# Kernel tuning notes

Hardware: AMD Instinct MI355X
Metric: run time of the kernel (lower is better)

Reference implementation:

```python
import jax, jax.numpy as jnp
import numpy as np

H = 768            # hidden_size
IMG_H = 1024       # image_hidden_size
NH = 12            # num_heads
NKV = 1            # num_kv_heads (MQA)
HD = H // NH       # head_dim = 64
FF = 4 * H         # intermediate_size = 3072
EPS = 1e-5


def layernorm(x, g, b):
    m = jnp.mean(x, axis=-1, keepdims=True)
    v = jnp.mean(jnp.square(x - m), axis=-1, keepdims=True)
    return (x - m) * jax.lax.rsqrt(v + EPS) * g + b


def setup_inputs() -> dict:
    key = jax.random.key(0)
    ks = jax.random.split(key, 12)
    B, NQ, NIMG = 8, 256, 4096
    s = 0.02
    return {
        "hidden_states": jax.random.normal(ks[0], (B, NQ, H), jnp.float32),
        "image_features": jax.random.normal(ks[1], (B, NIMG, IMG_H), jnp.float32),
        # norm_image_pre
        "ln_img_g": jnp.ones((IMG_H,), jnp.float32),
        "ln_img_b": jnp.zeros((IMG_H,), jnp.float32),
        # image_bottleneck (bias=False)
        "W_bottle": jax.random.normal(ks[2], (IMG_H, H), jnp.float32) * s,
        # norm_hidden
        "ln_h_g": jnp.ones((H,), jnp.float32),
        "ln_h_b": jnp.zeros((H,), jnp.float32),
        # to_q
        "Wq": jax.random.normal(ks[3], (H, H), jnp.float32) * s,
        "bq": jnp.zeros((H,), jnp.float32),
        # to_kv: out = num_kv_heads * head_dim * 2
        "Wkv": jax.random.normal(ks[4], (H, 2 * NKV * HD), jnp.float32) * s,
        "bkv": jnp.zeros((2 * NKV * HD,), jnp.float32),
        # to_out
        "Wo": jax.random.normal(ks[5], (H, H), jnp.float32) * s,
        "bo": jnp.zeros((H,), jnp.float32),
        # attn_out_norm
        "ln_ao_g": jnp.ones((H,), jnp.float32),
        "ln_ao_b": jnp.zeros((H,), jnp.float32),
        # gate
        "gate_param": jnp.zeros((), jnp.float32),
        # ffn_norm
        "ln_f_g": jnp.ones((H,), jnp.float32),
        "ln_f_b": jnp.zeros((H,), jnp.float32),
        # ffn
        "W1": jax.random.normal(ks[6], (H, FF), jnp.float32) * s,
        "b1": jnp.zeros((FF,), jnp.float32),
        "W2": jax.random.normal(ks[7], (FF, H), jnp.float32) * s,
        "b2": jnp.zeros((H,), jnp.float32),
    }


def reference(hidden_states, image_features, ln_img_g, ln_img_b, W_bottle,
              ln_h_g, ln_h_b, Wq, bq, Wkv, bkv, Wo, bo, ln_ao_g, ln_ao_b,
              gate_param, ln_f_g, ln_f_b, W1, b1, W2, b2):
    B, NQ, _ = hidden_states.shape
    # image pre-norm + bottleneck
    img = layernorm(image_features, ln_img_g, ln_img_b)
    img = img @ W_bottle                                   # [B, Nimg, H]
    # query path
    q_in = layernorm(hidden_states, ln_h_g, ln_h_b)
    q = (q_in @ Wq + bq).reshape(B, NQ, NH, HD).transpose(0, 2, 1, 3)  # b h i d
    # kv path (MQA: single shared KV head)
    kv = (img @ Wkv + bkv).reshape(B, -1, 2, NKV, HD)
    k = kv[:, :, 0, 0, :]                                  # [B, Nimg, HD]
    v = kv[:, :, 1, 0, :]
    scale = 1.0 / np.sqrt(HD)
    # broadcast KV across heads instead of explicit repeat
    scores = jnp.einsum('bhid,bjd->bhij', q * scale, k)    # [B, NH, NQ, Nimg]
    attn = jax.nn.softmax(scores, axis=-1)                 # dropout is identity (eval)
    out = jnp.einsum('bhij,bjd->bhid', attn, v)
    out = out.transpose(0, 2, 1, 3).reshape(B, NQ, H)
    out = out @ Wo + bo
    out = layernorm(out, ln_ao_g, ln_ao_b)
    gate = jax.nn.sigmoid(gate_param)
    h = hidden_states + gate * out
    ffn_in = layernorm(h, ln_f_g, ln_f_b)
    ffn_out = jax.nn.gelu(ffn_in @ W1 + b1, approximate=False) @ W2 + b2
    return h + ffn_out
```

## Files before the change

### kernel.cpp

```cpp
#include <hip/hip_runtime.h>
#include <cstdint>

typedef unsigned short u16;
typedef __bf16 bf16_t;
typedef bf16_t bf16x8 __attribute__((ext_vector_type(8)));
typedef float f32x4 __attribute__((ext_vector_type(4)));

__device__ __forceinline__ float b2f(u16 v) {
  union { uint32_t u; float f; } c; c.u = ((uint32_t)v) << 16; return c.f;
}
__device__ __forceinline__ u16 f2b(float f) {
  union { float f; uint32_t u; } c; c.f = f;
  uint32_t lsb = (c.u >> 16) & 1u;
  return (u16)((c.u + 0x7fffu + lsb) >> 16);
}
__device__ __forceinline__ uint4 pack8(f32x4 a, f32x4 b) {
  union { uint4 v; u16 s[8]; } r;
  r.s[0] = f2b(a[0]); r.s[1] = f2b(a[1]); r.s[2] = f2b(a[2]); r.s[3] = f2b(a[3]);
  r.s[4] = f2b(b[0]); r.s[5] = f2b(b[1]); r.s[6] = f2b(b[2]); r.s[7] = f2b(b[3]);
  return r.v;
}
__device__ __forceinline__ uint32_t cvt_pk_bf16(float lo, float hi) {
  uint32_t r;
  asm("v_cvt_pk_bf16_f32 %0, %1, %2" : "=v"(r) : "v"(lo), "v"(hi));
  return r;
}
__device__ __forceinline__ void phase_barrier() {
  asm volatile("s_waitcnt lgkmcnt(0)" ::: "memory");
  __builtin_amdgcn_s_barrier();
  asm volatile("" ::: "memory");
}
__device__ __forceinline__ void vm_drain() {
  asm volatile("s_waitcnt vmcnt(0)" ::: "memory");
}
template <int N>
__device__ __forceinline__ void vmwait() {
  asm volatile("s_waitcnt vmcnt(%0)" :: "n"(N) : "memory");
}
__device__ __forceinline__ void gload_lds16(const u16* g, u16* l) {
  __builtin_amdgcn_global_load_lds((const __attribute__((address_space(1))) void*)g,
                                   (__attribute__((address_space(3))) void*)l, 16, 0, 0);
}
__device__ __forceinline__ int xcd_swizzle(int lid, int nwg) {
  int q = nwg >> 3, r = nwg & 7, x = lid & 7, s = lid >> 3;
  return (x < r ? x * (q + 1) : r * (q + 1) + (x - r) * q) + s;
}

__global__ __launch_bounds__(256) void transpose_f2b(const float* __restrict__ in,
                                                     u16* __restrict__ out, int R, int C) {
  __shared__ __align__(16) u16 tile[32][33];
  int tx = threadIdx.x & 31, ty = threadIdx.x >> 5;
  int c0 = blockIdx.x * 32, r0 = blockIdx.y * 32;
#pragma unroll
  for (int i = 0; i < 4; ++i) {
    int r = r0 + ty + i * 8, c = c0 + tx;
    if (r < R && c < C) tile[ty + i * 8][tx] = f2b(in[(size_t)r * C + c]);
  }
  __syncthreads();
#pragma unroll
  for (int i = 0; i < 4; ++i) {
    int oc = c0 + ty + i * 8, orr = r0 + tx;
    if (oc < C && orr < R) out[(size_t)oc * R + orr] = tile[tx][ty + i * 8];
  }
}

__global__ __launch_bounds__(256) void prep_wg(const u16* __restrict__ WT, const float* __restrict__ g,
                                               const float* __restrict__ b, u16* __restrict__ WgT,
                                               float* __restrict__ ucol, float* __restrict__ wcol,
                                               int K) {
  int n = blockIdx.x * 4 + (threadIdx.x >> 6);
  int lane = threadIdx.x & 63;
  const u16* src = WT + (size_t)n * K;
  u16* dst = WgT + (size_t)n * K;
  float su = 0.f, sw = 0.f;
  for (int k = lane; k < K; k += 64) {
    float wc = b2f(src[k]);
    float wg = g[k] * wc;
    dst[k] = f2b(wg);
    su += wg;
    sw += b[k] * wc;
  }
#pragma unroll
  for (int off = 32; off >= 1; off >>= 1) {
    su += __shfl_xor(su, off, 64);
    sw += __shfl_xor(sw, off, 64);
  }
  if (lane == 0) { ucol[n] = su; wcol[n] = sw; }
}

__global__ __launch_bounds__(256) void hs_prep(const float* __restrict__ hs, u16* __restrict__ out,
                                               float* __restrict__ rstdg, float* __restrict__ mrstdg) {
  int row = blockIdx.x * 4 + (threadIdx.x >> 6);
  int lane = threadIdx.x & 63;
  const float* x = hs + (size_t)row * 768;
  float v[12];
#pragma unroll
  for (int it = 0; it < 3; ++it) {
    int c = (lane + it * 64) * 4;
    f32x4 d = *(const f32x4*)(x + c);
    v[it * 4 + 0] = d[0]; v[it * 4 + 1] = d[1]; v[it * 4 + 2] = d[2]; v[it * 4 + 3] = d[3];
  }
  float s = 0.f, s2 = 0.f;
#pragma unroll
  for (int i = 0; i < 12; ++i) { s += v[i]; s2 += v[i] * v[i]; }
#pragma unroll
  for (int off = 32; off >= 1; off >>= 1) {
    s += __shfl_xor(s, off, 64);
    s2 += __shfl_xor(s2, off, 64);
  }
  float inv_n = 1.0f / 768.f;
  float mean = s * inv_n;
  float var = fmaxf(s2 * inv_n - mean * mean, 0.f);
  float rstd = rsqrtf(var + 1e-5f);
  if (lane == 0) { rstdg[row] = rstd; mrstdg[row] = mean * rstd; }
#pragma unroll
  for (int it = 0; it < 3; ++it) {
    int c = (lane + it * 64) * 4;
    uint2 po;
    po.x = (uint32_t)f2b(v[it * 4 + 0]) | ((uint32_t)f2b(v[it * 4 + 1]) << 16);
    po.y = (uint32_t)f2b(v[it * 4 + 2]) | ((uint32_t)f2b(v[it * 4 + 3]) << 16);
    *(uint2*)(out + (size_t)row * 768 + c) = po;
  }
}

__global__ __launch_bounds__(256) void ln_res(const u16* __restrict__ ao, const float* __restrict__ g,
                                              const float* __restrict__ bta,
                                              const float* __restrict__ hs,
                                              const float* __restrict__ gatep,
                                              float* __restrict__ hf, u16* __restrict__ hb,
                                              float* __restrict__ rstdg, float* __restrict__ mrstdg) {
  int row = blockIdx.x * 4 + (threadIdx.x >> 6);
  int lane = threadIdx.x & 63;
  const u16* xb = ao + (size_t)row * 768;
  float v[12];
#pragma unroll
  for (int it = 0; it < 3; ++it) {
    int c = (lane + it * 64) * 4;
    uint2 d = *(const uint2*)(xb + c);
    v[it * 4 + 0] = b2f(d.x & 0xffff); v[it * 4 + 1] = b2f(d.x >> 16);
    v[it * 4 + 2] = b2f(d.y & 0xffff); v[it * 4 + 3] = b2f(d.y >> 16);
  }
  float s = 0.f, s2 = 0.f;
#pragma unroll
  for (int i = 0; i < 12; ++i) { s += v[i]; s2 += v[i] * v[i]; }
#pragma unroll
  for (int off = 32; off >= 1; off >>= 1) {
    s += __shfl_xor(s, off, 64);
    s2 += __shfl_xor(s2, off, 64);
  }
  float inv_n = 1.0f / 768.f;
  float mean = s * inv_n;
  float var = fmaxf(s2 * inv_n - mean * mean, 0.f);
  float rstd = rsqrtf(var + 1e-5f);
  float gate = 1.f / (1.f + __expf(-gatep[0]));
  float hsum = 0.f, hsum2 = 0.f;
  float o[12];
#pragma unroll
  for (int it = 0; it < 3; ++it) {
    int c = (lane + it * 64) * 4;
    const float* rr = hs + (size_t)row * 768 + c;
#pragma unroll
    for (int i = 0; i < 4; ++i) {
      float hv = rr[i] + gate * ((v[it * 4 + i] - mean) * rstd * g[c + i] + bta[c + i]);
      o[it * 4 + i] = hv;
      hsum += hv; hsum2 += hv * hv;
    }
    *(f32x4*)(hf + (size_t)row * 768 + c) = (f32x4){o[it * 4 + 0], o[it * 4 + 1], o[it * 4 + 2], o[it * 4 + 3]};
    uint2 po;
    po.x = (uint32_t)f2b(o[it * 4 + 0]) | ((uint32_t)f2b(o[it * 4 + 1]) << 16);
    po.y = (uint32_t)f2b(o[it * 4 + 2]) | ((uint32_t)f2b(o[it * 4 + 3]) << 16);
    *(uint2*)(hb + (size_t)row * 768 + c) = po;
  }
#pragma unroll
  for (int off = 32; off >= 1; off >>= 1) {
    hsum += __shfl_xor(hsum, off, 64);
    hsum2 += __shfl_xor(hsum2, off, 64);
  }
  float hm = hsum * inv_n;
  float hvar = fmaxf(hsum2 * inv_n - hm * hm, 0.f);
  float hrstd = rsqrtf(hvar + 1e-5f);
  if (lane == 0) { rstdg[row] = hrstd; mrstdg[row] = hm * hrstd; }
}

template <int BM, int SPLITK, int AMODE, int BMODE, int EPI, bool OUTF32, bool VTOUT>
__device__ __forceinline__ void gemm_body(const void* __restrict__ Av, const void* __restrict__ Bv,
                                          const float* __restrict__ bias,
                                          const float* __restrict__ rstdg,
                                          const float* __restrict__ mrstdg,
                                          const float* __restrict__ ucol,
                                          const float* __restrict__ wcol,
                                          void* __restrict__ Cv, u16* __restrict__ VTout,
                                          int M, int N, int K) {
  constexpr int MT = BM / 32;
  constexpr int AL = BM / 64;
  constexpr bool PURE = (AMODE == 0 && BMODE == 0);
  constexpr int NBUF = PURE ? 4 : 2;
  constexpr int LPT = AL + 2;
  __shared__ __align__(16) u16 aT[NBUF][BM * 32];
  __shared__ __align__(16) u16 bT[NBUF][128 * 32];
  __shared__ float rstd_s[EPI == 4 ? 128 : 1];
  __shared__ float mrstd_s[EPI == 4 ? 128 : 1];
  __shared__ __align__(16) u16 vtile[VTOUT ? 64 * 136 : 1];

  int gx = gridDim.x, gy = gridDim.y;
  int nwg = gx * gy * (int)gridDim.z;
  int lid = ((int)blockIdx.z * gy + (int)blockIdx.y) * gx + (int)blockIdx.x;
  int wid = xcd_swizzle(lid, nwg);
  int bz = wid / (gx * gy);
  int rem = wid - bz * (gx * gy);
  int bx = rem / gy;
  int by = rem - bx * gy;

  int t = threadIdx.x, lane = t & 63, wave = t >> 6;
  int quad = lane >> 4, lcol = lane & 15;
  int wm = (wave >> 1) * (16 * MT), wn = (wave & 1) * 64;
  const u16* Ab = (const u16*)Av;
  const float* Af = (const float*)Av;
  const u16* Bb = (const u16*)Bv;
  const float* Bf = (const float*)Bv;
  const int kchunk = (SPLITK > 1) ? K / SPLITK : K;
  const int kstart = (SPLITK > 1) ? bz * kchunk : 0;
  int rr = t >> 1, rc = t & 1;
  float sa = 0.f, sa2 = 0.f;
  f32x4 acc[MT][4];
#pragma unroll
  for (int i = 0; i < MT; ++i)
#pragma unroll
    for (int j = 0; j < 4; ++j) acc[i][j] = (f32x4){0.f, 0.f, 0.f, 0.f};

  f32x4 araw[4], braw[4];

  auto dmaA = [&](int buf, int k0) {
#pragma unroll
    for (int s2 = 0; s2 < AL; ++s2) {
      int row = (wave * AL + s2) * 16 + (lane >> 2);
      int ch = (lane & 3) ^ (row & 3);
      gload_lds16(Ab + (size_t)(bx * BM + row) * K + kstart + k0 + ch * 8,
                  &aT[buf][(wave * AL + s2) * 512]);
    }
  };
  auto dmaB = [&](int buf, int k0) {
#pragma unroll
    for (int s2 = 0; s2 < 2; ++s2) {
      int row = (wave * 2 + s2) * 16 + (lane >> 2);
      int ch = (lane & 3) ^ (row & 3);
      gload_lds16(Bb + (size_t)(by * 128 + row) * K + kstart + k0 + ch * 8,
                  &bT[buf][(wave * 2 + s2) * 512]);
    }
  };
  auto regloadA = [&](int k0) {
    const f32x4* p = (const f32x4*)&Af[(size_t)(bx * BM + rr) * K + kstart + k0 + rc * 16];
#pragma unroll
    for (int i = 0; i < 4; ++i) araw[i] = p[i];
  };
  auto regstoreA = [&](int buf) {
    if (EPI == 4) {
#pragma unroll
      for (int i = 0; i < 4; ++i)
#pragma unroll
        for (int j = 0; j < 4; ++j) { sa += araw[i][j]; sa2 += araw[i][j] * araw[i][j]; }
    }
    uint4 c0 = pack8(araw[0], araw[1]), c1 = pack8(araw[2], araw[3]);
    *(uint4*)&aT[buf][rr * 32 + (((rc * 2 + 0) ^ (rr & 3)) << 3)] = c0;
    *(uint4*)&aT[buf][rr * 32 + (((rc * 2 + 1) ^ (rr & 3)) << 3)] = c1;
  };
  auto regloadB = [&](int k0) {
    const f32x4* p = (const f32x4*)&Bf[(size_t)(by * 128 + rr) * K + kstart + k0 + rc * 16];
#pragma unroll
    for (int i = 0; i < 4; ++i) braw[i] = p[i];
  };
  auto regstoreB = [&](int buf) {
    uint4 c0 = pack8(braw[0], braw[1]), c1 = pack8(braw[2], braw[3]);
    *(uint4*)&bT[buf][rr * 32 + (((rc * 2 + 0) ^ (rr & 3)) << 3)] = c0;
    *(uint4*)&bT[buf][rr * 32 + (((rc * 2 + 1) ^ (rr & 3)) << 3)] = c1;
  };
  auto compute = [&](int buf) {
    bf16x8 af[MT], bfr[4];
#pragma unroll
    for (int mt = 0; mt < MT; ++mt) {
      int r = wm + mt * 16 + lcol;
      af[mt] = *(const bf16x8*)&aT[buf][r * 32 + (((quad ^ (r & 3))) << 3)];
    }
#pragma unroll
    for (int nt = 0; nt < 4; ++nt) {
      int r = wn + nt * 16 + lcol;
      bfr[nt] = *(const bf16x8*)&bT[buf][r * 32 + (((quad ^ (r & 3))) << 3)];
    }
#pragma unroll
    for (int mt = 0; mt < MT; ++mt)
#pragma unroll
      for (int nt = 0; nt < 4; ++nt)
        acc[mt][nt] = __builtin_amdgcn_mfma_f32_16x16x32_bf16(af[mt], bfr[nt], acc[mt][nt], 0, 0, 0);
  };

  const int nk = kchunk >> 5;
  if (PURE) {
    dmaA(0, 0); dmaB(0, 0);
    if (nk > 1) { dmaA(1, 1 << 5); dmaB(1, 1 << 5); }
    if (nk > 2) { dmaA(2, 2 << 5); dmaB(2, 2 << 5); }
    for (int kt = 0; kt < nk; ++kt) {
      int left = nk - 1 - kt;
      if (left >= 2) vmwait<2 * LPT>();
      else if (left == 1) vmwait<LPT>();
      else vmwait<0>();
      phase_barrier();
      if (kt + 3 < nk) { dmaA((kt + 3) & 3, (kt + 3) << 5); dmaB((kt + 3) & 3, (kt + 3) << 5); }
      compute(kt & 3);
    }
  } else {
    if (AMODE == 1) regloadA(0); else dmaA(0, 0);
    if (BMODE == 1) regloadB(0); else dmaB(0, 0);
    if (AMODE == 1) regstoreA(0);
    if (BMODE == 1) regstoreB(0);
    vm_drain();
    phase_barrier();
    int cur = 0;
    for (int kt = 0; kt < nk; ++kt) {
      bool more = kt + 1 < nk;
      if (more) {
        if (AMODE == 1) regloadA((kt + 1) << 5); else dmaA(cur ^ 1, (kt + 1) << 5);
        if (BMODE == 1) regloadB((kt + 1) << 5); else dmaB(cur ^ 1, (kt + 1) << 5);
      }
      compute(cur);
      if (more) {
        if (AMODE == 1) regstoreA(cur ^ 1);
        if (BMODE == 1) regstoreB(cur ^ 1);
      }
      vm_drain();
      phase_barrier();
      cur ^= 1;
    }
  }

  if (EPI == 4) {
    float s = sa, s2 = sa2;
    s += __shfl_xor(s, 1, 64);
    s2 += __shfl_xor(s2, 1, 64);
    if ((t & 1) == 0) {
      float inv_n = 1.0f / (float)K;
      float mean = s * inv_n;
      float var = fmaxf(s2 * inv_n - mean * mean, 0.f);
      float rstd = rsqrtf(var + 1e-5f);
      rstd_s[rr] = rstd;
      mrstd_s[rr] = mean * rstd;
    }
    __syncthreads();
  }

  if (VTOUT) {
    u16* kb = (u16*)Cv;
#pragma unroll
    for (int mt = 0; mt < MT; ++mt) {
#pragma unroll
      for (int nt = 0; nt < 4; ++nt) {
#pragma unroll
        for (int r = 0; r < 4; ++r) {
          int lrow = wm + mt * 16 + quad * 4 + r;
          int row = bx * BM + lrow;
          int col = wn + nt * 16 + lcol;
          float v = rstd_s[lrow] * acc[mt][nt][r] - mrstd_s[lrow] * ucol[col] + wcol[col] + bias[col];
          u16 hv = f2b(v);
          if (wn == 0) kb[(size_t)row * 64 + col] = hv;
          else vtile[(col - 64) * 136 + lrow] = hv;
        }
      }
    }
    __syncthreads();
    int dd = t >> 2, js = (t & 3) * 32;
    int bg = bx >> 5, j0g = (bx & 31) * 128;
    u16* dst = VTout + ((size_t)bg * 64 + dd) * 4096 + j0g + js;
#pragma unroll
    for (int i = 0; i < 4; ++i)
      *(uint4*)(dst + i * 8) = *(const uint4*)&vtile[dd * 136 + js + i * 8];
    return;
  }

  u16* Cb = (u16*)Cv;
  float* Cf = (float*)Cv;
  if (SPLITK > 1) Cf += (size_t)bz * (size_t)M * (size_t)N;
#pragma unroll
  for (int mt = 0; mt < MT; ++mt) {
#pragma unroll
    for (int nt = 0; nt < 4; ++nt) {
#pragma unroll
      for (int r = 0; r < 4; ++r) {
        int lrow = wm + mt * 16 + quad * 4 + r;
        int row = bx * BM + lrow;
        int col = by * 128 + wn + nt * 16 + lcol;
        float v = acc[mt][nt][r];
        if (EPI == 1) v += bias[col];
        if (EPI == 3 || EPI == 5)
          v = rstdg[row] * v - mrstdg[row] * ucol[col] + wcol[col] + bias[col];
        if (EPI == 5) v = 0.5f * v * (1.f + erff(v * 0.70710678118f));
        size_t idx = (size_t)row * N + col;
        if (OUTF32) Cf[idx] = v; else Cb[idx] = f2b(v);
      }
    }
  }
}

#define GEMM_ARGS const void* Av, const void* Bv, const float* bias, const float* rstdg, \
                  const float* mrstdg, const float* ucol, const float* wcol, void* Cv,   \
                  u16* VTout, int M, int N, int K
__global__ __launch_bounds__(256) void gemm_wc(GEMM_ARGS) {
  gemm_body<128, 1, 0, 1, 0, false, false>(Av, Bv, bias, rstdg, mrstdg, ucol, wcol, Cv, VTout, M, N, K);
}
__global__ __launch_bounds__(256) void gemm_kv(GEMM_ARGS) {
  gemm_body<128, 1, 1, 0, 4, false, true>(Av, Bv, bias, rstdg, mrstdg, ucol, wcol, Cv, VTout, M, N, K);
}
__global__ __launch_bounds__(256) void gemm_q(GEMM_ARGS) {
  gemm_body<64, 1, 0, 0, 3, false, false>(Av, Bv, bias, rstdg, mrstdg, ucol, wcol, Cv, VTout, M, N, K);
}
__global__ __launch_bounds__(256) void gemm_o(GEMM_ARGS) {
  gemm_body<64, 1, 0, 0, 1, false, false>(Av, Bv, bias, rstdg, mrstdg, ucol, wcol, Cv, VTout, M, N, K);
}
__global__ __launch_bounds__(256) void gemm_w1(GEMM_ARGS) {
  gemm_body<128, 1, 0, 0, 5, false, false>(Av, Bv, bias, rstdg, mrstdg, ucol, wcol, Cv, VTout, M, N, K);
}
__global__ __launch_bounds__(256) void gemm_w2(GEMM_ARGS) {
  gemm_body<64, 2, 0, 0, 0, true, false>(Av, Bv, bias, rstdg, mrstdg, ucol, wcol, Cv, VTout, M, N, K);
}

__global__ __launch_bounds__(256) void w2_merge(const float* __restrict__ part,
                                                const float* __restrict__ hf,
                                                const float* __restrict__ b2,
                                                float* __restrict__ out) {
  int idx = blockIdx.x * 256 + threadIdx.x;
  f32x4 p0 = ((const f32x4*)part)[idx];
  f32x4 p1 = ((const f32x4*)part)[idx + 393216];
  f32x4 h = ((const f32x4*)hf)[idx];
  f32x4 bb = ((const f32x4*)b2)[idx % 192];
  f32x4 o;
#pragma unroll
  for (int i = 0; i < 4; ++i) o[i] = p0[i] + p1[i] + h[i] + bb[i];
  ((f32x4*)out)[idx] = o;
}

__global__ __launch_bounds__(256) void attn_kernel(const u16* __restrict__ qbuf,
                                                   const u16* __restrict__ kb,
                                                   const u16* __restrict__ VT,
                                                   float* __restrict__ Opart,
                                                   float* __restrict__ lpart) {
  __shared__ __align__(16) u16 k_lds[2][64 * 72];
  __shared__ __align__(16) u16 vt_lds[2][64 * 72];
  __shared__ __align__(16) u16 p_lds[4 * 16 * 72];
  int lid = ((int)blockIdx.z * 12 + (int)blockIdx.y) * 4 + (int)blockIdx.x;
  int wid = (lid & 7) * 192 + (lid >> 3);
  int bi = wid & 3;
  int h = (wid >> 2) % 12;
  int z = wid / 48;
  int b = z >> 2, s = z & 3;
  int t = threadIdx.x;
  int wave = t >> 6, lane = t & 63, quad = lane >> 4, lcol = lane & 15;
  int i0 = bi * 64 + wave * 16;
  const u16* qrow = qbuf + ((size_t)(b * 256 + i0 + lcol) * 768 + h * 64 + quad * 8);
  bf16x8 qf0 = *(const bf16x8*)qrow;
  bf16x8 qf1 = *(const bf16x8*)(qrow + 32);
  float l_r[4] = {0.f, 0.f, 0.f, 0.f};
  f32x4 oacc[4];
#pragma unroll
  for (int nt = 0; nt < 4; ++nt) oacc[nt] = (f32x4){0.f, 0.f, 0.f, 0.f};
  int sr = t >> 2, sc = (t & 3) * 16;
  const u16* kbase = kb + (size_t)b * 4096 * 64;
  const u16* vtbase = VT + (size_t)b * 64 * 4096;
  u16* pw = &p_lds[wave * 16 * 72];

  uint4 kr0, kr1, vr0, vr1;
  auto stage_load = [&](int jt) {
    int j0 = s * 1024 + jt * 64;
    const u16* krow = kbase + (size_t)(j0 + sr) * 64 + sc;
    kr0 = *(const uint4*)(krow);
    kr1 = *(const uint4*)(krow + 8);
    const u16* vrow = vtbase + (size_t)sr * 4096 + j0 + sc;
    vr0 = *(const uint4*)(vrow);
    vr1 = *(const uint4*)(vrow + 8);
  };
  auto stage_store = [&](int buf) {
    *(uint4*)&k_lds[buf][sr * 72 + sc] = kr0;
    *(uint4*)&k_lds[buf][sr * 72 + sc + 8] = kr1;
    *(uint4*)&vt_lds[buf][sr * 72 + sc] = vr0;
    *(uint4*)&vt_lds[buf][sr * 72 + sc + 8] = vr1;
  };

  stage_load(0);
  stage_store(0);
  phase_barrier();
  int cur = 0;
  for (int jt = 0; jt < 16; ++jt) {
    bool more = jt + 1 < 16;
    if (more) stage_load(jt + 1);

    f32x4 sc4[4];
#pragma unroll
    for (int nt = 0; nt < 4; ++nt) sc4[nt] = (f32x4){0.f, 0.f, 0.f, 0.f};
    __builtin_amdgcn_s_setprio(1);
#pragma unroll
    for (int nt = 0; nt < 4; ++nt) {
      bf16x8 kb0 = *(const bf16x8*)&k_lds[cur][(nt * 16 + lcol) * 72 + quad * 8];
      bf16x8 kb1 = *(const bf16x8*)&k_lds[cur][(nt * 16 + lcol) * 72 + 32 + quad * 8];
      sc4[nt] = __builtin_amdgcn_mfma_f32_16x16x32_bf16(qf0, kb0, sc4[nt], 0, 0, 0);
      sc4[nt] = __builtin_amdgcn_mfma_f32_16x16x32_bf16(qf1, kb1, sc4[nt], 0, 0, 0);
    }
    __builtin_amdgcn_s_setprio(0);
#pragma unroll
    for (int r = 0; r < 4; ++r) {
      float rsum = 0.f;
#pragma unroll
      for (int nt = 0; nt < 4; ++nt) {
        float p = __expf(sc4[nt][r] * 0.125f);
        sc4[nt][r] = p;
        rsum += p;
      }
      rsum += __shfl_xor(rsum, 1, 64);
      rsum += __shfl_xor(rsum, 2, 64);
      rsum += __shfl_xor(rsum, 4, 64);
      rsum += __shfl_xor(rsum, 8, 64);
      l_r[r] += rsum;
      uint32_t pk01 = cvt_pk_bf16(sc4[0][r], sc4[1][r]);
      uint32_t pk23 = cvt_pk_bf16(sc4[2][r], sc4[3][r]);
      int prow = (quad * 4 + r) * 72 + lcol;
      pw[prow] = (u16)(pk01 & 0xffff);
      pw[prow + 16] = (u16)(pk01 >> 16);
      pw[prow + 32] = (u16)(pk23 & 0xffff);
      pw[prow + 48] = (u16)(pk23 >> 16);
    }
    __builtin_amdgcn_s_setprio(1);
#pragma unroll
    for (int ks = 0; ks < 2; ++ks) {
      bf16x8 pa = *(const bf16x8*)&pw[lcol * 72 + ks * 32 + quad * 8];
#pragma unroll
      for (int nt = 0; nt < 4; ++nt) {
        bf16x8 vb = *(const bf16x8*)&vt_lds[cur][(nt * 16 + lcol) * 72 + ks * 32 + quad * 8];
        oacc[nt] = __builtin_amdgcn_mfma_f32_16x16x32_bf16(pa, vb, oacc[nt], 0, 0, 0);
      }
    }
    __builtin_amdgcn_s_setprio(0);
    if (more) stage_store(cur ^ 1);
    phase_barrier();
    cur ^= 1;
  }
  size_t base = ((size_t)z * 12 + h) * 256;
#pragma unroll
  for (int r = 0; r < 4; ++r) {
    int row = bi * 64 + wave * 16 + quad * 4 + r;
#pragma unroll
    for (int nt = 0; nt < 4; ++nt)
      Opart[(base + row) * 64 + nt * 16 + lcol] = oacc[nt][r];
    if (lcol == 0) lpart[base + row] = l_r[r];
  }
}

__global__ __launch_bounds__(256) void attn_merge(const float* __restrict__ Opart,
                                                  const float* __restrict__ lpart,
                                                  u16* __restrict__ attn_o) {
  int row = blockIdx.x;
  int col = blockIdx.y * 256 + threadIdx.x;
  int b = row >> 8, i = row & 255, h = col >> 6, d = col & 63;
  float o = 0.f, l = 0.f;
#pragma unroll
  for (int s = 0; s < 4; ++s) {
    size_t ii = (((size_t)(b * 4 + s) * 12 + h) * 256 + i);
    o += Opart[ii * 64 + d];
    l += lpart[ii];
  }
  attn_o[(size_t)row * 768 + col] = f2b(o / l);
}

extern "C" void kernel_launch(void* const* d_in, const int* in_sizes, int n_in, void* d_out,
                              int out_size, void* d_ws, size_t ws_size, hipStream_t stream) {
  (void)in_sizes; (void)n_in; (void)out_size; (void)ws_size;
  const float* hs = (const float*)d_in[0];
  const float* imgf = (const float*)d_in[1];
  const float* ln_img_g = (const float*)d_in[2];
  const float* ln_img_b = (const float*)d_in[3];
  const float* W_bottle = (const float*)d_in[4];
  const float* ln_h_g = (const float*)d_in[5];
  const float* ln_h_b = (const float*)d_in[6];
  const float* Wq = (const float*)d_in[7];
  const float* bq = (const float*)d_in[8];
  const float* Wkv = (const float*)d_in[9];
  const float* bkv = (const float*)d_in[10];
  const float* Wo = (const float*)d_in[11];
  const float* bo = (const float*)d_in[12];
  const float* ln_ao_g = (const float*)d_in[13];
  const float* ln_ao_b = (const float*)d_in[14];
  const float* gatep = (const float*)d_in[15];
  const float* ln_f_g = (const float*)d_in[16];
  const float* ln_f_b = (const float*)d_in[17];
  const float* W1 = (const float*)d_in[18];
  const float* b1 = (const float*)d_in[19];
  const float* W2 = (const float*)d_in[20];
  const float* b2 = (const float*)d_in[21];

  char* sc = (char*)d_ws;
  auto alloc = [&](size_t bytes) {
    char* p = sc;
    sc += (bytes + 63) & ~(size_t)63;
    return p;
  };
  u16* WTq = (u16*)alloc(768 * 768 * 2);
  u16* WTo = (u16*)alloc(768 * 768 * 2);
  u16* WT1 = (u16*)alloc(3072 * 768 * 2);
  u16* WT2 = (u16*)alloc(768 * 3072 * 2);
  u16* WkvT = (u16*)alloc(128 * 768 * 2);
  u16* WcT = (u16*)alloc(128 * 1024 * 2);
  u16* WgT = (u16*)alloc(128 * 1024 * 2);
  u16* WqgT = (u16*)alloc(768 * 768 * 2);
  u16* W1gT = (u16*)alloc(3072 * 768 * 2);
  float* ucol = (float*)alloc(128 * 4);
  float* wcol = (float*)alloc(128 * 4);
  float* uq = (float*)alloc(768 * 4);
  float* wq = (float*)alloc(768 * 4);
  float* u1 = (float*)alloc(3072 * 4);
  float* w1c = (float*)alloc(3072 * 4);
  float* rstdq = (float*)alloc(2048 * 4);
  float* mrstdq = (float*)alloc(2048 * 4);
  float* rstdh = (float*)alloc(2048 * 4);
  float* mrstdh = (float*)alloc(2048 * 4);
  u16* hs16 = (u16*)alloc(2048 * 768 * 2);
  u16* kb = (u16*)alloc((size_t)32768 * 64 * 2);
  u16* VT = (u16*)alloc((size_t)8 * 64 * 4096 * 2);
  u16* qb = (u16*)alloc(2048 * 768 * 2);
  u16* attn_o = (u16*)alloc(2048 * 768 * 2);
  u16* ao = (u16*)alloc(2048 * 768 * 2);
  u16* hbuf = (u16*)alloc(2048 * 768 * 2);
  float* hf32 = (float*)alloc(2048 * 768 * 4);
  u16* actb = (u16*)alloc((size_t)2048 * 3072 * 2);
  float* Opart = (float*)alloc((size_t)32 * 12 * 256 * 64 * 4);
  float* lpart = (float*)alloc((size_t)32 * 12 * 256 * 4);

  transpose_f2b<<<dim3(24, 24), 256, 0, stream>>>(Wq, WTq, 768, 768);
  transpose_f2b<<<dim3(24, 24), 256, 0, stream>>>(Wo, WTo, 768, 768);
  transpose_f2b<<<dim3(96, 24), 256, 0, stream>>>(W1, WT1, 768, 3072);
  transpose_f2b<<<dim3(24, 96), 256, 0, stream>>>(W2, WT2, 3072, 768);
  transpose_f2b<<<dim3(4, 24), 256, 0, stream>>>(Wkv, WkvT, 768, 128);

  gemm_wc<<<dim3(1, 8), 256, 0, stream>>>(WkvT, W_bottle, nullptr, nullptr, nullptr, nullptr,
                                          nullptr, WcT, nullptr, 128, 1024, 768);
  prep_wg<<<32, 256, 0, stream>>>(WcT, ln_img_g, ln_img_b, WgT, ucol, wcol, 1024);
  prep_wg<<<192, 256, 0, stream>>>(WTq, ln_h_g, ln_h_b, WqgT, uq, wq, 768);
  prep_wg<<<768, 256, 0, stream>>>(WT1, ln_f_g, ln_f_b, W1gT, u1, w1c, 768);
  hs_prep<<<512, 256, 0, stream>>>(hs, hs16, rstdq, mrstdq);
  gemm_kv<<<dim3(256, 1), 256, 0, stream>>>(imgf, WgT, bkv, nullptr, nullptr, ucol, wcol,
                                            kb, VT, 32768, 128, 1024);
  gemm_q<<<dim3(32, 6), 256, 0, stream>>>(hs16, WqgT, bq, rstdq, mrstdq, uq, wq,
                                          qb, nullptr, 2048, 768, 768);
  attn_kernel<<<dim3(4, 12, 32), 256, 0, stream>>>(qb, kb, VT, Opart, lpart);
  attn_merge<<<dim3(2048, 3), 256, 0, stream>>>(Opart, lpart, attn_o);
  gemm_o<<<dim3(32, 6), 256, 0, stream>>>(attn_o, WTo, bo, nullptr, nullptr, nullptr, nullptr,
                                          ao, nullptr, 2048, 768, 768);
  ln_res<<<512, 256, 0, stream>>>(ao, ln_ao_g, ln_ao_b, hs, gatep, hf32, hbuf, rstdh, mrstdh);
  gemm_w1<<<dim3(16, 24), 256, 0, stream>>>(hbuf, W1gT, b1, rstdh, mrstdh, u1, w1c,
                                            actb, nullptr, 2048, 3072, 768);
  gemm_w2<<<dim3(32, 6, 2), 256, 0, stream>>>(actb, WT2, nullptr, nullptr, nullptr, nullptr, nullptr,
                                              Opart, nullptr, 2048, 768, 3072);
  w2_merge<<<1536, 256, 0, stream>>>(Opart, hf32, b2, (float*)d_out);
}
```

Measured before the change: 522.3 us.

## Batch prep kernels, pre-convert image rows, pair heads in attention, retile W2

Result: slower. 532.9 us (+2.0%).

```diff
diff --git a/kernel.cpp b/kernel.cpp
--- a/kernel.cpp
+++ b/kernel.cpp
@@ -46,22 +46,61 @@
   return (x < r ? x * (q + 1) : r * (q + 1) + (x - r) * q) + s;
 }
 
-__global__ __launch_bounds__(256) void transpose_f2b(const float* __restrict__ in,
-                                                     u16* __restrict__ out, int R, int C) {
+__global__ __launch_bounds__(256) void transpose_all(
+    const float* __restrict__ Wq, const float* __restrict__ Wo, const float* __restrict__ W1,
+    const float* __restrict__ W2, const float* __restrict__ Wkv,
+    u16* __restrict__ WTq, u16* __restrict__ WTo, u16* __restrict__ WT1,
+    u16* __restrict__ WT2, u16* __restrict__ WkvT) {
   __shared__ __align__(16) u16 tile[32][33];
+  int bid = blockIdx.x;
+  const float* in; u16* out; int R, C, gx, tb;
+  if (bid < 576)       { in = Wq;  out = WTq;  R = 768;  C = 768;  gx = 24; tb = bid; }
+  else if (bid < 1152) { in = Wo;  out = WTo;  R = 768;  C = 768;  gx = 24; tb = bid - 576; }
+  else if (bid < 3456) { in = W1;  out = WT1;  R = 768;  C = 3072; gx = 96; tb = bid - 1152; }
+  else if (bid < 5760) { in = W2;  out = WT2;  R = 3072; C = 768;  gx = 24; tb = bid - 3456; }
+  else                 { in = Wkv; out = WkvT; R = 768;  C = 128;  gx = 4;  tb = bid - 5760; }
+  int c0 = (tb % gx) * 32, r0 = (tb / gx) * 32;
   int tx = threadIdx.x & 31, ty = threadIdx.x >> 5;
-  int c0 = blockIdx.x * 32, r0 = blockIdx.y * 32;
 #pragma unroll
   for (int i = 0; i < 4; ++i) {
     int r = r0 + ty + i * 8, c = c0 + tx;
-    if (r < R && c < C) tile[ty + i * 8][tx] = f2b(in[(size_t)r * C + c]);
+    tile[ty + i * 8][tx] = f2b(in[(size_t)r * C + c]);
   }
   __syncthreads();
 #pragma unroll
   for (int i = 0; i < 4; ++i) {
     int oc = c0 + ty + i * 8, orr = r0 + tx;
-    if (oc < C && orr < R) out[(size_t)oc * R + orr] = tile[tx][ty + i * 8];
-  }
+    out[(size_t)oc * R + orr] = tile[tx][ty + i * 8];
+  }
+}
+
+__global__ __launch_bounds__(256) void prep_wg2(
+    const u16* __restrict__ WTq, const float* __restrict__ gq, const float* __restrict__ bq_,
+    u16* __restrict__ WqgT, float* __restrict__ uq, float* __restrict__ wq,
+    const u16* __restrict__ WT1, const float* __restrict__ g1, const float* __restrict__ b1_,
+    u16* __restrict__ W1gT, float* __restrict__ u1, float* __restrict__ w1) {
+  int bid = blockIdx.x;
+  const u16* WT; const float* g; const float* b; u16* WgT; float* u; float* w; int n0;
+  if (bid < 192) { WT = WTq; g = gq; b = bq_; WgT = WqgT; u = uq; w = wq; n0 = bid * 4; }
+  else { WT = WT1; g = g1; b = b1_; WgT = W1gT; u = u1; w = w1; n0 = (bid - 192) * 4; }
+  int n = n0 + (threadIdx.x >> 6);
+  int lane = threadIdx.x & 63;
+  const u16* src = WT + (size_t)n * 768;
+  u16* dst = WgT + (size_t)n * 768;
+  float su = 0.f, sw = 0.f;
+  for (int k = lane; k < 768; k += 64) {
+    float wc = b2f(src[k]);
+    float wg = g[k] * wc;
+    dst[k] = f2b(wg);
+    su += wg;
+    sw += b[k] * wc;
+  }
+#pragma unroll
+  for (int off = 32; off >= 1; off >>= 1) {
+    su += __shfl_xor(su, off, 64);
+    sw += __shfl_xor(sw, off, 64);
+  }
+  if (lane == 0) { u[n] = su; w[n] = sw; }
 }
 
 __global__ __launch_bounds__(256) void prep_wg(const u16* __restrict__ WT, const float* __restrict__ g,
@@ -88,38 +127,72 @@
   if (lane == 0) { ucol[n] = su; wcol[n] = sw; }
 }
 
-__global__ __launch_bounds__(256) void hs_prep(const float* __restrict__ hs, u16* __restrict__ out,
-                                               float* __restrict__ rstdg, float* __restrict__ mrstdg) {
-  int row = blockIdx.x * 4 + (threadIdx.x >> 6);
-  int lane = threadIdx.x & 63;
-  const float* x = hs + (size_t)row * 768;
-  float v[12];
-#pragma unroll
-  for (int it = 0; it < 3; ++it) {
-    int c = (lane + it * 64) * 4;
-    f32x4 d = *(const f32x4*)(x + c);
-    v[it * 4 + 0] = d[0]; v[it * 4 + 1] = d[1]; v[it * 4 + 2] = d[2]; v[it * 4 + 3] = d[3];
-  }
-  float s = 0.f, s2 = 0.f;
-#pragma unroll
-  for (int i = 0; i < 12; ++i) { s += v[i]; s2 += v[i] * v[i]; }
-#pragma unroll
-  for (int off = 32; off >= 1; off >>= 1) {
-    s += __shfl_xor(s, off, 64);
-    s2 += __shfl_xor(s2, off, 64);
-  }
-  float inv_n = 1.0f / 768.f;
-  float mean = s * inv_n;
-  float var = fmaxf(s2 * inv_n - mean * mean, 0.f);
-  float rstd = rsqrtf(var + 1e-5f);
-  if (lane == 0) { rstdg[row] = rstd; mrstdg[row] = mean * rstd; }
-#pragma unroll
-  for (int it = 0; it < 3; ++it) {
-    int c = (lane + it * 64) * 4;
-    uint2 po;
-    po.x = (uint32_t)f2b(v[it * 4 + 0]) | ((uint32_t)f2b(v[it * 4 + 1]) << 16);
-    po.y = (uint32_t)f2b(v[it * 4 + 2]) | ((uint32_t)f2b(v[it * 4 + 3]) << 16);
-    *(uint2*)(out + (size_t)row * 768 + c) = po;
+__global__ __launch_bounds__(256) void rowprep(
+    const float* __restrict__ hs, u16* __restrict__ hs16,
+    float* __restrict__ rstdq, float* __restrict__ mrstdq,
+    const float* __restrict__ img, u16* __restrict__ img16,
+    float* __restrict__ rstdi, float* __restrict__ mrstdi) {
+  int bid = blockIdx.x, w = threadIdx.x >> 6, lane = threadIdx.x & 63;
+  if (bid < 512) {
+    int row = bid * 4 + w;
+    const float* x = hs + (size_t)row * 768;
+    float v[12];
+#pragma unroll
+    for (int it = 0; it < 3; ++it) {
+      f32x4 d = *(const f32x4*)(x + (lane + it * 64) * 4);
+      v[it * 4 + 0] = d[0]; v[it * 4 + 1] = d[1]; v[it * 4 + 2] = d[2]; v[it * 4 + 3] = d[3];
+    }
+    float s = 0.f, s2 = 0.f;
+#pragma unroll
+    for (int i = 0; i < 12; ++i) { s += v[i]; s2 += v[i] * v[i]; }
+#pragma unroll
+    for (int off = 32; off >= 1; off >>= 1) {
+      s += __shfl_xor(s, off, 64);
+      s2 += __shfl_xor(s2, off, 64);
+    }
+    float inv_n = 1.0f / 768.f;
+    float mean = s * inv_n;
+    float var = fmaxf(s2 * inv_n - mean * mean, 0.f);
+    float rstd = rsqrtf(var + 1e-5f);
+    if (lane == 0) { rstdq[row] = rstd; mrstdq[row] = mean * rstd; }
+#pragma unroll
+    for (int it = 0; it < 3; ++it) {
+      int c = (lane + it * 64) * 4;
+      uint2 po;
+      po.x = (uint32_t)f2b(v[it * 4 + 0]) | ((uint32_t)f2b(v[it * 4 + 1]) << 16);
+      po.y = (uint32_t)f2b(v[it * 4 + 2]) | ((uint32_t)f2b(v[it * 4 + 3]) << 16);
+      *(uint2*)(hs16 + (size_t)row * 768 + c) = po;
+    }
+  } else {
+    int row = (bid - 512) * 4 + w;
+    const float* x = img + (size_t)row * 1024;
+    float v[16];
+#pragma unroll
+    for (int it = 0; it < 4; ++it) {
+      f32x4 d = *(const f32x4*)(x + (lane + it * 64) * 4);
+      v[it * 4 + 0] = d[0]; v[it * 4 + 1] = d[1]; v[it * 4 + 2] = d[2]; v[it * 4 + 3] = d[3];
+    }
+    float s = 0.f, s2 = 0.f;
+#pragma unroll
+    for (int i = 0; i < 16; ++i) { s += v[i]; s2 += v[i] * v[i]; }
+#pragma unroll
+    for (int off = 32; off >= 1; off >>= 1) {
+      s += __shfl_xor(s, off, 64);
+      s2 += __shfl_xor(s2, off, 64);
+    }
+    float inv_n = 1.0f / 1024.f;
+    float mean = s * inv_n;
+    float var = fmaxf(s2 * inv_n - mean * mean, 0.f);
+    float rstd = rsqrtf(var + 1e-5f);
+    if (lane == 0) { rstdi[row] = rstd; mrstdi[row] = mean * rstd; }
+#pragma unroll
+    for (int it = 0; it < 4; ++it) {
+      int c = (lane + it * 64) * 4;
+      uint2 po;
+      po.x = (uint32_t)f2b(v[it * 4 + 0]) | ((uint32_t)f2b(v[it * 4 + 1]) << 16);
+      po.y = (uint32_t)f2b(v[it * 4 + 2]) | ((uint32_t)f2b(v[it * 4 + 3]) << 16);
+      *(uint2*)(img16 + (size_t)row * 1024 + c) = po;
+    }
   }
 }
 
@@ -198,9 +271,6 @@
   constexpr int LPT = AL + 2;
   __shared__ __align__(16) u16 aT[NBUF][BM * 32];
   __shared__ __align__(16) u16 bT[NBUF][128 * 32];
-  __shared__ float rstd_s[EPI == 4 ? 128 : 1];
-  __shared__ float mrstd_s[EPI == 4 ? 128 : 1];
-  __shared__ __align__(16) u16 vtile[VTOUT ? 64 * 136 : 1];
 
   int gx = gridDim.x, gy = gridDim.y;
   int nwg = gx * gy * (int)gridDim.z;
@@ -215,20 +285,18 @@
   int quad = lane >> 4, lcol = lane & 15;
   int wm = (wave >> 1) * (16 * MT), wn = (wave & 1) * 64;
   const u16* Ab = (const u16*)Av;
-  const float* Af = (const float*)Av;
   const u16* Bb = (const u16*)Bv;
   const float* Bf = (const float*)Bv;
   const int kchunk = (SPLITK > 1) ? K / SPLITK : K;
   const int kstart = (SPLITK > 1) ? bz * kchunk : 0;
   int rr = t >> 1, rc = t & 1;
-  float sa = 0.f, sa2 = 0.f;
   f32x4 acc[MT][4];
 #pragma unroll
   for (int i = 0; i < MT; ++i)
 #pragma unroll
     for (int j = 0; j < 4; ++j) acc[i][j] = (f32x4){0.f, 0.f, 0.f, 0.f};
 
-  f32x4 araw[4], braw[4];
+  f32x4 braw[4];
 
   auto dmaA = [&](int buf, int k0) {
 #pragma unroll
@@ -247,22 +315,6 @@
       gload_lds16(Bb + (size_t)(by * 128 + row) * K + kstart + k0 + ch * 8,
                   &bT[buf][(wave * 2 + s2) * 512]);
     }
-  };
-  auto regloadA = [&](int k0) {
-    const f32x4* p = (const f32x4*)&Af[(size_t)(bx * BM + rr) * K + kstart + k0 + rc * 16];
-#pragma unroll
-    for (int i = 0; i < 4; ++i) araw[i] = p[i];
-  };
-  auto regstoreA = [&](int buf) {
-    if (EPI == 4) {
-#pragma unroll
-      for (int i = 0; i < 4; ++i)
-#pragma unroll
-        for (int j = 0; j < 4; ++j) { sa += araw[i][j]; sa2 += araw[i][j] * araw[i][j]; }
-    }
-    uint4 c0 = pack8(araw[0], araw[1]), c1 = pack8(araw[2], araw[3]);
-    *(uint4*)&aT[buf][rr * 32 + (((rc * 2 + 0) ^ (rr & 3)) << 3)] = c0;
-    *(uint4*)&aT[buf][rr * 32 + (((rc * 2 + 1) ^ (rr & 3)) << 3)] = c1;
   };
   auto regloadB = [&](int k0) {
     const f32x4* p = (const f32x4*)&Bf[(size_t)(by * 128 + rr) * K + kstart + k0 + rc * 16];
@@ -308,46 +360,26 @@
       compute(kt & 3);
     }
   } else {
-    if (AMODE == 1) regloadA(0); else dmaA(0, 0);
-    if (BMODE == 1) regloadB(0); else dmaB(0, 0);
-    if (AMODE == 1) regstoreA(0);
-    if (BMODE == 1) regstoreB(0);
+    dmaA(0, 0);
+    regloadB(0);
+    regstoreB(0);
     vm_drain();
     phase_barrier();
     int cur = 0;
     for (int kt = 0; kt < nk; ++kt) {
       bool more = kt + 1 < nk;
-      if (more) {
-        if (AMODE == 1) regloadA((kt + 1) << 5); else dmaA(cur ^ 1, (kt + 1) << 5);
-        if (BMODE == 1) regloadB((kt + 1) << 5); else dmaB(cur ^ 1, (kt + 1) << 5);
-      }
+      if (more) { dmaA(cur ^ 1, (kt + 1) << 5); regloadB((kt + 1) << 5); }
       compute(cur);
-      if (more) {
-        if (AMODE == 1) regstoreA(cur ^ 1);
-        if (BMODE == 1) regstoreB(cur ^ 1);
-      }
+      if (more) regstoreB(cur ^ 1);
       vm_drain();
       phase_barrier();
       cur ^= 1;
     }
   }
 
-  if (EPI == 4) {
-    float s = sa, s2 = sa2;
-    s += __shfl_xor(s, 1, 64);
-    s2 += __shfl_xor(s2, 1, 64);
-    if ((t & 1) == 0) {
-      float inv_n = 1.0f / (float)K;
-      float mean = s * inv_n;
-      float var = fmaxf(s2 * inv_n - mean * mean, 0.f);
-      float rstd = rsqrtf(var + 1e-5f);
-      rstd_s[rr] = rstd;
-      mrstd_s[rr] = mean * rstd;
-    }
+  if (VTOUT) {
     __syncthreads();
-  }
-
-  if (VTOUT) {
+    u16* vtile = &aT[0][0];
     u16* kb = (u16*)Cv;
 #pragma unroll
     for (int mt = 0; mt < MT; ++mt) {
@@ -358,7 +390,7 @@
           int lrow = wm + mt * 16 + quad * 4 + r;
           int row = bx * BM + lrow;
           int col = wn + nt * 16 + lcol;
-          float v = rstd_s[lrow] * acc[mt][nt][r] - mrstd_s[lrow] * ucol[col] + wcol[col] + bias[col];
+          float v = rstdg[row] * acc[mt][nt][r] - mrstdg[row] * ucol[col] + wcol[col] + bias[col];
           u16 hv = f2b(v);
           if (wn == 0) kb[(size_t)row * 64 + col] = hv;
           else vtile[(col - 64) * 136 + lrow] = hv;
@@ -406,7 +438,7 @@
   gemm_body<128, 1, 0, 1, 0, false, false>(Av, Bv, bias, rstdg, mrstdg, ucol, wcol, Cv, VTout, M, N, K);
 }
 __global__ __launch_bounds__(256) void gemm_kv(GEMM_ARGS) {
-  gemm_body<128, 1, 1, 0, 4, false, true>(Av, Bv, bias, rstdg, mrstdg, ucol, wcol, Cv, VTout, M, N, K);
+  gemm_body<128, 1, 0, 0, 3, false, true>(Av, Bv, bias, rstdg, mrstdg, ucol, wcol, Cv, VTout, M, N, K);
 }
 __global__ __launch_bounds__(256) void gemm_q(GEMM_ARGS) {
   gemm_body<64, 1, 0, 0, 3, false, false>(Av, Bv, bias, rstdg, mrstdg, ucol, wcol, Cv, VTout, M, N, K);
@@ -418,7 +450,7 @@
   gemm_body<128, 1, 0, 0, 5, false, false>(Av, Bv, bias, rstdg, mrstdg, ucol, wcol, Cv, VTout, M, N, K);
 }
 __global__ __launch_bounds__(256) void gemm_w2(GEMM_ARGS) {
-  gemm_body<64, 2, 0, 0, 0, true, false>(Av, Bv, bias, rstdg, mrstdg, ucol, wcol, Cv, VTout, M, N, K);
+  gemm_body<128, 2, 0, 0, 0, true, false>(Av, Bv, bias, rstdg, mrstdg, ucol, wcol, Cv, VTout, M, N, K);
 }
 
 __global__ __launch_bounds__(256) void w2_merge(const float* __restrict__ part,
@@ -444,22 +476,28 @@
   __shared__ __align__(16) u16 k_lds[2][64 * 72];
   __shared__ __align__(16) u16 vt_lds[2][64 * 72];
   __shared__ __align__(16) u16 p_lds[4 * 16 * 72];
-  int lid = ((int)blockIdx.z * 12 + (int)blockIdx.y) * 4 + (int)blockIdx.x;
-  int wid = (lid & 7) * 192 + (lid >> 3);
+  int lid = ((int)blockIdx.z * 6 + (int)blockIdx.y) * 4 + (int)blockIdx.x;
+  int wid = (lid & 7) * 96 + (lid >> 3);
   int bi = wid & 3;
-  int h = (wid >> 2) % 12;
-  int z = wid / 48;
+  int hp = (wid >> 2) % 6;
+  int z = wid / 24;
   int b = z >> 2, s = z & 3;
   int t = threadIdx.x;
   int wave = t >> 6, lane = t & 63, quad = lane >> 4, lcol = lane & 15;
   int i0 = bi * 64 + wave * 16;
-  const u16* qrow = qbuf + ((size_t)(b * 256 + i0 + lcol) * 768 + h * 64 + quad * 8);
-  bf16x8 qf0 = *(const bf16x8*)qrow;
-  bf16x8 qf1 = *(const bf16x8*)(qrow + 32);
-  float l_r[4] = {0.f, 0.f, 0.f, 0.f};
-  f32x4 oacc[4];
-#pragma unroll
-  for (int nt = 0; nt < 4; ++nt) oacc[nt] = (f32x4){0.f, 0.f, 0.f, 0.f};
+  bf16x8 qf[2][2];
+#pragma unroll
+  for (int h2 = 0; h2 < 2; ++h2) {
+    const u16* qrow = qbuf + ((size_t)(b * 256 + i0 + lcol) * 768 + (hp * 2 + h2) * 64 + quad * 8);
+    qf[h2][0] = *(const bf16x8*)qrow;
+    qf[h2][1] = *(const bf16x8*)(qrow + 32);
+  }
+  float l_r[2][4] = {{0.f, 0.f, 0.f, 0.f}, {0.f, 0.f, 0.f, 0.f}};
+  f32x4 oacc[2][4];
+#pragma unroll
+  for (int h2 = 0; h2 < 2; ++h2)
+#pragma unroll
+    for (int nt = 0; nt < 4; ++nt) oacc[h2][nt] = (f32x4){0.f, 0.f, 0.f, 0.f};
   int sr = t >> 2, sc = (t & 3) * 16;
   const u16* kbase = kb + (size_t)b * 4096 * 64;
   const u16* vtbase = VT + (size_t)b * 64 * 4096;
@@ -490,63 +528,69 @@
     bool more = jt + 1 < 16;
     if (more) stage_load(jt + 1);
 
-    f32x4 sc4[4];
-#pragma unroll
-    for (int nt = 0; nt < 4; ++nt) sc4[nt] = (f32x4){0.f, 0.f, 0.f, 0.f};
-    __builtin_amdgcn_s_setprio(1);
-#pragma unroll
-    for (int nt = 0; nt < 4; ++nt) {
-      bf16x8 kb0 = *(const bf16x8*)&k_lds[cur][(nt * 16 + lcol) * 72 + quad * 8];
-      bf16x8 kb1 = *(const bf16x8*)&k_lds[cur][(nt * 16 + lcol) * 72 + 32 + quad * 8];
-      sc4[nt] = __builtin_amdgcn_mfma_f32_16x16x32_bf16(qf0, kb0, sc4[nt], 0, 0, 0);
-      sc4[nt] = __builtin_amdgcn_mfma_f32_16x16x32_bf16(qf1, kb1, sc4[nt], 0, 0, 0);
-    }
-    __builtin_amdgcn_s_setprio(0);
-#pragma unroll
-    for (int r = 0; r < 4; ++r) {
-      float rsum = 0.f;
+#pragma unroll
+    for (int h2 = 0; h2 < 2; ++h2) {
+      f32x4 sc4[4];
+#pragma unroll
+      for (int nt = 0; nt < 4; ++nt) sc4[nt] = (f32x4){0.f, 0.f, 0.f, 0.f};
+      __builtin_amdgcn_s_setprio(1);
 #pragma unroll
       for (int nt = 0; nt < 4; ++nt) {
-        float p = __expf(sc4[nt][r] * 0.125f);
-        sc4[nt][r] = p;
-        rsum += p;
+        bf16x8 kb0 = *(const bf16x8*)&k_lds[cur][(nt * 16 + lcol) * 72 + quad * 8];
+        bf16x8 kb1 = *(const bf16x8*)&k_lds[cur][(nt * 16 + lcol) * 72 + 32 + quad * 8];
+        sc4[nt] = __builtin_amdgcn_mfma_f32_16x16x32_bf16(qf[h2][0], kb0, sc4[nt], 0, 0, 0);
+        sc4[nt] = __builtin_amdgcn_mfma_f32_16x16x32_bf16(qf[h2][1], kb1, sc4[nt], 0, 0, 0);
       }
-      rsum += __shfl_xor(rsum, 1, 64);
-      rsum += __shfl_xor(rsum, 2, 64);
-      rsum += __shfl_xor(rsum, 4, 64);
-      rsum += __shfl_xor(rsum, 8, 64);
-      l_r[r] += rsum;
-      uint32_t pk01 = cvt_pk_bf16(sc4[0][r], sc4[1][r]);
-      uint32_t pk23 = cvt_pk_bf16(sc4[2][r], sc4[3][r]);
-      int prow = (quad * 4 + r) * 72 + lcol;
-      pw[prow] = (u16)(pk01 & 0xffff);
-      pw[prow + 16] = (u16)(pk01 >> 16);
-      pw[prow + 32] = (u16)(pk23 & 0xffff);
-      pw[prow + 48] = (u16)(pk23 >> 16);
-    }
-    __builtin_amdgcn_s_setprio(1);
-#pragma unroll
-    for (int ks = 0; ks < 2; ++ks) {
-      bf16x8 pa = *(const bf16x8*)&pw[lcol * 72 + ks * 32 + quad * 8];
-#pragma unroll
-      for (int nt = 0; nt < 4; ++nt) {
-        bf16x8 vb = *(const bf16x8*)&vt_lds[cur][(nt * 16 + lcol) * 72 + ks * 32 + quad * 8];
-        oacc[nt] = __builtin_amdgcn_mfma_f32_16x16x32_bf16(pa, vb, oacc[nt], 0, 0, 0);
+      __builtin_amdgcn_s_setprio(0);
+#pragma unroll
+      for (int r = 0; r < 4; ++r) {
+        float rsum = 0.f;
+#pragma unroll
+        for (int nt = 0; nt < 4; ++nt) {
+          float p = __expf(sc4[nt][r] * 0.125f);
+          sc4[nt][r] = p;
+          rsum += p;
+        }
+        rsum += __shfl_xor(rsum, 1, 64);
+        rsum += __shfl_xor(rsum, 2, 64);
+        rsum += __shfl_xor(rsum, 4, 64);
+        rsum += __shfl_xor(rsum, 8, 64);
+        l_r[h2][r] += rsum;
+        uint32_t pk01 = cvt_pk_bf16(sc4[0][r], sc4[1][r]);
+        uint32_t pk23 = cvt_pk_bf16(sc4[2][r], sc4[3][r]);
+        int prow = (quad * 4 + r) * 72 + lcol;
+        pw[prow] = (u16)(pk01 & 0xffff);
+        pw[prow + 16] = (u16)(pk01 >> 16);
+        pw[prow + 32] = (u16)(pk23 & 0xffff);
+        pw[prow + 48] = (u16)(pk23 >> 16);
       }
-    }
-    __builtin_amdgcn_s_setprio(0);
+      __builtin_amdgcn_s_setprio(1);
+#pragma unroll
+      for (int ks = 0; ks < 2; ++ks) {
+        bf16x8 pa = *(const bf16x8*)&pw[lcol * 72 + ks * 32 + quad * 8];
+#pragma unroll
+        for (int nt = 0; nt < 4; ++nt) {
+          bf16x8 vb = *(const bf16x8*)&vt_lds[cur][(nt * 16 + lcol) * 72 + ks * 32 + quad * 8];
+          oacc[h2][nt] = __builtin_amdgcn_mfma_f32_16x16x32_bf16(pa, vb, oacc[h2][nt], 0, 0, 0);
+        }
+      }
+      __builtin_amdgcn_s_setprio(0);
+    }
     if (more) stage_store(cur ^ 1);
     phase_barrier();
     cur ^= 1;
   }
-  size_t base = ((size_t)z * 12 + h) * 256;
-#pragma unroll
-  for (int r = 0; r < 4; ++r) {
-    int row = bi * 64 + wave * 16 + quad * 4 + r;
-#pragma unroll
-    for (int nt = 0; nt < 4; ++nt)
-      Opart[(base + row) * 64 + nt * 16 + lcol] = oacc[nt][r];
-    if (lcol == 0) lpart[base + row] = l_r[r];
+#pragma unroll
+  for (int h2 = 0; h2 < 2; ++h2) {
+    size_t base = ((size_t)z * 12 + hp * 2 + h2) * 256;
+#pragma unroll
+    for (int r = 0; r < 4; ++r) {
+      int row = bi * 64 + wave * 16 + quad * 4 + r;
+#pragma unroll
+      for (int nt = 0; nt < 4; ++nt)
+        Opart[(base + row) * 64 + nt * 16 + lcol] = oacc[h2][nt][r];
+      if (lcol == 0) lpart[base + row] = l_r[h2][r];
+    }
   }
 }
 
@@ -617,7 +661,10 @@
   float* mrstdq = (float*)alloc(2048 * 4);
   float* rstdh = (float*)alloc(2048 * 4);
   float* mrstdh = (float*)alloc(2048 * 4);
+  float* rstdi = (float*)alloc(32768 * 4);
+  float* mrstdi = (float*)alloc(32768 * 4);
   u16* hs16 = (u16*)alloc(2048 * 768 * 2);
+  u16* img16 = (u16*)alloc((size_t)32768 * 1024 * 2);
   u16* kb = (u16*)alloc((size_t)32768 * 64 * 2);
   u16* VT = (u16*)alloc((size_t)8 * 64 * 4096 * 2);
   u16* qb = (u16*)alloc(2048 * 768 * 2);
@@ -629,30 +676,25 @@
   float* Opart = (float*)alloc((size_t)32 * 12 * 256 * 64 * 4);
   float* lpart = (float*)alloc((size_t)32 * 12 * 256 * 4);
 
-  transpose_f2b<<<dim3(24, 24), 256, 0, stream>>>(Wq, WTq, 768, 768);
-  transpose_f2b<<<dim3(24, 24), 256, 0, stream>>>(Wo, WTo, 768, 768);
-  transpose_f2b<<<dim3(96, 24), 256, 0, stream>>>(W1, WT1, 768, 3072);
-  transpose_f2b<<<dim3(24, 96), 256, 0, stream>>>(W2, WT2, 3072, 768);
-  transpose_f2b<<<dim3(4, 24), 256, 0, stream>>>(Wkv, WkvT, 768, 128);
-
+  transpose_all<<<5856, 256, 0, stream>>>(Wq, Wo, W1, W2, Wkv, WTq, WTo, WT1, WT2, WkvT);
+  prep_wg2<<<960, 256, 0, stream>>>(WTq, ln_h_g, ln_h_b, WqgT, uq, wq,
+                                    WT1, ln_f_g, ln_f_b, W1gT, u1, w1c);
   gemm_wc<<<dim3(1, 8), 256, 0, stream>>>(WkvT, W_bottle, nullptr, nullptr, nullptr, nullptr,
                                           nullptr, WcT, nullptr, 128, 1024, 768);
   prep_wg<<<32, 256, 0, stream>>>(WcT, ln_img_g, ln_img_b, WgT, ucol, wcol, 1024);
-  prep_wg<<<192, 256, 0, stream>>>(WTq, ln_h_g, ln_h_b, WqgT, uq, wq, 768);
-  prep_wg<<<768, 256, 0, stream>>>(WT1, ln_f_g, ln_f_b, W1gT, u1, w1c, 768);
-  hs_prep<<<512, 256, 0, stream>>>(hs, hs16, rstdq, mrstdq);
-  gemm_kv<<<dim3(256, 1), 256, 0, stream>>>(imgf, WgT, bkv, nullptr, nullptr, ucol, wcol,
+  rowprep<<<8704, 256, 0, stream>>>(hs, hs16, rstdq, mrstdq, imgf, img16, rstdi, mrstdi);
+  gemm_kv<<<dim3(256, 1), 256, 0, stream>>>(img16, WgT, bkv, rstdi, mrstdi, ucol, wcol,
                                             kb, VT, 32768, 128, 1024);
   gemm_q<<<dim3(32, 6), 256, 0, stream>>>(hs16, WqgT, bq, rstdq, mrstdq, uq, wq,
                                           qb, nullptr, 2048, 768, 768);
-  attn_kernel<<<dim3(4, 12, 32), 256, 0, stream>>>(qb, kb, VT, Opart, lpart);
+  attn_kernel<<<dim3(4, 6, 32), 256, 0, stream>>>(qb, kb, VT, Opart, lpart);
   attn_merge<<<dim3(2048, 3), 256, 0, stream>>>(Opart, lpart, attn_o);
   gemm_o<<<dim3(32, 6), 256, 0, stream>>>(attn_o, WTo, bo, nullptr, nullptr, nullptr, nullptr,
                                           ao, nullptr, 2048, 768, 768);
   ln_res<<<512, 256, 0, stream>>>(ao, ln_ao_g, ln_ao_b, hs, gatep, hf32, hbuf, rstdh, mrstdh);
   gemm_w1<<<dim3(16, 24), 256, 0, stream>>>(hbuf, W1gT, b1, rstdh, mrstdh, u1, w1c,
                                             actb, nullptr, 2048, 3072, 768);
-  gemm_w2<<<dim3(32, 6, 2), 256, 0, stream>>>(actb, WT2, nullptr, nullptr, nullptr, nullptr, nullptr,
+  gemm_w2<<<dim3(16, 6, 2), 256, 0, stream>>>(actb, WT2, nullptr, nullptr, nullptr, nullptr, nullptr,
                                               Opart, nullptr, 2048, 768, 3072);
   w2_merge<<<1536, 256, 0, stream>>>(Opart, hf32, b2, (float*)d_out);
 }
```
